# Kernel tuning notes

Measured on AMD Instinct MI355X. Metric: run time of the kernel, lower is better.

Reference implementation:

```python
import jax, jax.numpy as jnp
import numpy as np

ALPHA, BETA, GAMMA = 1.0, 1.0, 0.7
WIN = 11
C1 = 0.01 ** 2
C2 = 0.03 ** 2


def get_sobel_kernels(n1=1, n2=2, n3=2):
    a = np.asarray
    Sx = a([[[-n1, 0, n1], [-n2, 0, n2], [-n1, 0, n1]],
            [[-n2, 0, n2], [-n3 * n2, 0, n3 * n2], [-n2, 0, n2]],
            [[-n1, 0, n1], [-n2, 0, n2], [-n1, 0, n1]]])
    Sy = a([[[-n1, -n2, -n1], [0, 0, 0], [n1, n2, n1]],
            [[-n2, -n3 * n2, -n2], [0, 0, 0], [n2, n3 * n2, n2]],
            [[-n1, -n2, -n1], [0, 0, 0], [n1, n2, n1]]])
    Sz = a([[[-n1, -n2, -n1], [-n2, -n3 * n2, -n2], [-n1, -n2, -n1]],
            [[0, 0, 0], [0, 0, 0], [0, 0, 0]],
            [[n1, n2, n1], [n2, n3 * n2, n2], [n1, n2, n1]]])
    Sd11 = a([[[0, n1, n2], [-n1, 0, n1], [-n2, -n1, 0]],
              [[0, n2, n2 * n3], [-n2, 0, n2], [-n2 * n3, -n2, 0]],
              [[0, n1, n2], [-n1, 0, n1], [-n2, -n1, 0]]])
    Sd12 = a([[[-n2, -n1, 0], [-n1, 0, n1], [0, n1, n2]],
              [[-n2 * n3, -n2, 0], [-n2, 0, n2], [0, n2, n2 * n3]],
              [[-n2, -n1, 0], [-n1, 0, n1], [0, n1, n2]]])
    Sd21 = Sd11.T
    Sd22 = Sd12.T
    Sd31 = a([-S.T for S in Sd11.T])
    Sd32 = a([S.T for S in Sd12.T])
    return np.stack([Sx, Sy, Sz, Sd11, Sd12, Sd21, Sd22, Sd31, Sd32]).astype(np.float32)

# (9,1,3,3,3) fused sobel bank -- single grouped conv instead of 9 launches
SOBEL_W = jnp.asarray(get_sobel_kernels()[:, None])


def _gauss1d():
    g = jnp.exp(-(jnp.arange(WIN, dtype=jnp.float32) - WIN // 2) ** 2 / (2 * 1.5 ** 2))
    return g / g.sum()

G1D = _gauss1d()


def conv3d(x, w):
    return jax.lax.conv_general_dilated(
        x, w, window_strides=(1, 1, 1), padding='SAME',
        dimension_numbers=('NCDHW', 'OIDHW', 'NCDHW'))


def gauss_filter(x):
    # separable 11-tap gaussian along D, H, W (== full 11^3 window, zero-padded SAME)
    x = conv3d(x, G1D.reshape(1, 1, WIN, 1, 1))
    x = conv3d(x, G1D.reshape(1, 1, 1, WIN, 1))
    x = conv3d(x, G1D.reshape(1, 1, 1, 1, WIN))
    return x


def edge_map(img):
    # GradEdge3D.__call__ with a=1, C=1
    B, C, D, H, W = img.shape
    xp = jnp.pad(img, ((0, 0), (0, 0), (1, 1), (1, 1), (1, 1)), mode='reflect')
    g = conv3d(xp, SOBEL_W)                       # (B, 9, D+2, H+2, W+2)
    gm = jnp.sqrt(jnp.sum((g + 1e-6) ** 2 + 1e-6, axis=1))  # (B, D+2, H+2, W+2)
    gm = gm[:, 1:-1, 1:-1, 1:-1]
    norm = (gm - gm.min()) / (gm.max() - gm.min() + 1e-6)
    return norm.reshape(B, 1, D, H, W)


def ssim_value(pred, target):
    mu_p = gauss_filter(pred)
    mu_t = gauss_filter(target)
    mu_p2, mu_t2, mu_pt = mu_p ** 2, mu_t ** 2, mu_p * mu_t
    sig_p = gauss_filter(pred * pred) - mu_p2
    sig_t = gauss_filter(target * target) - mu_t2
    sig_pt = gauss_filter(pred * target) - mu_pt
    ssim_map = ((2 * mu_pt + C1) * (2 * sig_pt + C2)) / ((mu_p2 + mu_t2 + C1) * (sig_p + sig_t + C2))
    return 1.0 - ssim_map.mean()


def setup_inputs() -> dict:
    key = jax.random.key(0)
    k1, k2 = jax.random.split(key)
    shape = (2, 1, 128, 128, 128)
    return {
        'pred': jax.random.uniform(k1, shape, dtype=jnp.float32),
        'target': jax.random.uniform(k2, shape, dtype=jnp.float32),
    }


def reference(pred, target):
    loss_mse = jnp.mean((pred - target) ** 2)
    loss_ssim = ssim_value(pred, target)
    # GMELoss3D: lam_errors=[(1.0, L1Loss())], reduction='sum'
    loss_gme = 1e-6 + jnp.mean(jnp.abs(edge_map(pred) - edge_map(target)))
    total = ALPHA * loss_mse + BETA * loss_ssim + GAMMA * loss_gme
    return (total, loss_mse, loss_ssim, loss_gme)
```

## Files before the change

### kernel.cpp

```cpp
#include <hip/hip_runtime.h>


#define VOL 4194304
#define HV  2097152

typedef _Float16 h2 __attribute__((ext_vector_type(2)));
typedef _Float16 h4 __attribute__((ext_vector_type(4)));
typedef _Float16 h8 __attribute__((ext_vector_type(8)));

constexpr float GW[11] = {
    0.00102838f, 0.00759876f, 0.03600077f, 0.10936070f, 0.21300554f,
    0.26601173f,
    0.21300554f, 0.10936070f, 0.03600077f, 0.00759876f, 0.00102838f};



__device__ __forceinline__ void wblur_body(
    const float* __restrict__ p, const float* __restrict__ t,
    _Float16* __restrict__ A, double* __restrict__ mseB, const int bidx) {
  __shared__ float sr[2][138];
  __shared__ float dr[2][138];
  __shared__ float redw[256];
  const int tid = threadIdx.x;
  const int rl = tid >> 7;
  const int x  = tid & 127;
  const int rowBase = bidx << 4;
  if (x < 5)    { sr[rl][x] = 0.f;      dr[rl][x] = 0.f; }
  if (x >= 123) { sr[rl][10 + x] = 0.f; dr[rl][10 + x] = 0.f; }
  float pv = p[((rowBase + rl) << 7) + x];
  float tv = t[((rowBase + rl) << 7) + x];
  float msel = 0.f;
  h4* __restrict__ A4 = (h4*)A;
  for (int it = 0; it < 8; ++it) {
    const int row  = rowBase + (it << 1) + rl;
    const int base = row << 7;
    const float sv = pv + tv;
    const float dv = pv - tv;
    sr[rl][5 + x] = sv; dr[rl][5 + x] = dv;
    msel += dv * dv;
    __syncthreads();
    float pvN = 0.f, tvN = 0.f;
    if (it < 7) {
      const int baseN = (row + 2) << 7;
      pvN = p[baseN + x]; tvN = t[baseN + x];
    }
    float as = 0.f, ad = 0.f, ass = 0.f, add_ = 0.f;
#pragma unroll
    for (int k = 0; k < 11; ++k) {
      const float w = GW[k];
      const float a = sr[rl][x + k];
      const float b = dr[rl][x + k];
      const float wa = w * a;
      const float wb = w * b;
      as += wa; ad += wb;
      ass += wa * a; add_ += wb * b;
    }
    h4 o;
    o[0] = (_Float16)as;  o[1] = (_Float16)ad;
    o[2] = (_Float16)ass; o[3] = (_Float16)add_;
    A4[base + x] = o;
    __syncthreads();
    pv = pvN; tv = tvN;
  }
  redw[tid] = msel;
  __syncthreads();
  for (int s = 128; s > 0; s >>= 1) {
    if (tid < s) redw[tid] += redw[tid + s];
    __syncthreads();
  }
  if (tid == 0) atomicAdd(&mseB[(bidx & 63) << 3], (double)redw[0]);
}

__device__ __forceinline__ void sobel_body(
    const float* __restrict__ p, const float* __restrict__ t,
    _Float16* __restrict__ gmP, _Float16* __restrict__ gmT,
    unsigned int* __restrict__ ui, const int bx, const int by, const int bz) {
  __shared__ float sb[1296];
  __shared__ float rmin[256];
  __shared__ float rmax[256];
  const int tid = threadIdx.x;
  const int tx = tid & 15;
  const int ty = tid >> 4;
  const int x0 = bx << 4;
  const int y0 = by << 4;
  const int vol = bz >> 3;
  const int b   = (bz >> 2) & 1;
  const int z0  = (bz & 3) << 5;
  const float* __restrict__ img = vol ? t : p;
  _Float16* __restrict__ gm = vol ? gmT : gmP;
  const int vb = b << 21;

  const int ly1 = tid / 24, lx1 = tid % 24;
  const bool v1 = (lx1 < 18);
  int gy1 = y0 - 1 + ly1; gy1 = gy1 < 0 ? 1 : (gy1 > 127 ? 126 : gy1);
  int gx1 = x0 - 1 + lx1; gx1 = gx1 < 0 ? 1 : (gx1 > 127 ? 126 : gx1);
  const int off1 = (gy1 << 7) + gx1;
  const int s2i = tid + 256;
  const int ly2 = s2i / 24, lx2 = s2i % 24;
  const bool v2 = (s2i < 432) && (lx2 < 18);
  int gy2 = y0 - 1 + ly2; gy2 = gy2 < 0 ? 1 : (gy2 > 127 ? 126 : gy2);
  int gx2 = x0 - 1 + lx2; gx2 = gx2 < 0 ? 1 : (gx2 > 127 ? 126 : gx2);
  const int off2 = (gy2 << 7) + gx2;
  const int rb = ty * 24 + tx;
  const int gbase = vb + (z0 << 14) + ((y0 + ty) << 7) + (x0 + tx);

  float Y0[7], Y1[7], Y2[7];
  float rv1 = 0.f, rv2 = 0.f;
  float lmin = 3.4e38f, lmax = 0.f;

#define LOADR(ZS) {                                                         \
    const int zc_ = (ZS) > 127 ? 126 : (ZS);                                \
    const int za_ = vb + (zc_ << 14);                                       \
    if (v1) rv1 = img[za_ + off1];                                          \
    if (v2) rv2 = img[za_ + off2]; }

#define WRITELDS(BOFF) {                                                    \
    if (v1) sb[(BOFF) + tid] = rv1;                                         \
    if (v2) sb[(BOFF) + s2i] = rv2; }

#define COMPY(P) {                                                          \
    const int o_ = (P) * 432 + rb;                                          \
    const float r00 = sb[o_],      r01 = sb[o_ + 1],  r02 = sb[o_ + 2];     \
    const float r10 = sb[o_ + 24], r11 = sb[o_ + 25], r12 = sb[o_ + 26];    \
    const float r20 = sb[o_ + 48], r21 = sb[o_ + 49], r22 = sb[o_ + 50];    \
    const float dx0 = r02 - r00, dx1 = r12 - r10, dx2 = r22 - r20;          \
    const float ux0 = r00 + r01 + r02, ux1 = r10 + r11 + r12,               \
                ux2 = r20 + r21 + r22;                                      \
    const float sx0 = ux0 + r01, sx1 = ux1 + r11, sx2 = ux2 + r21;          \
    Y##P[1] = dx0 + dx1 + dx2;                                    \
    Y##P[0] = Y##P[1] + dx1;                                      \
    Y##P[2] = sx2 - sx0;                                          \
    Y##P[4] = sx0 + sx1 + sx2;                                    \
    Y##P[3] = Y##P[4] + sx1;                                      \
    Y##P[5] = ux2 - ux0;                                          \
    Y##P[6] = (ux0 + ux2) + 2.f * ux1; }

#define EMIT(I, P0, P1, P2) {                                               \
    const float E_ = Y##P0[0] + Y##P1[0] + Y##P2[0];                        \
    const float g1 = E_ + Y##P1[0];                                         \
    const float tA = Y##P0[1] + Y##P1[1] + Y##P2[1];                        \
    const float A_ = tA + Y##P1[1];                                         \
    const float D_ = Y##P0[2] + Y##P1[2] + Y##P2[2];                        \
    const float g2 = D_ + Y##P1[2];                                         \
    const float g3 = Y##P2[3] - Y##P0[3];                                   \
    const float C_ = Y##P2[4] - Y##P0[4];                                   \
    const float B_ = (Y##P0[5] + Y##P2[5]) + 2.f * Y##P1[5];                \
    const float F_ = Y##P2[6] - Y##P0[6];                                   \
    const float g4 = A_ - B_, g5 = A_ + B_;                                 \
    const float g6 = C_ - D_, g7 = C_ + D_;                                 \
    const float g8 = E_ - F_, g9 = E_ + F_;                                 \
    float ss_ = 9e-6f, t_;                                                  \
    t_ = g1 + 1e-6f; ss_ = fmaf(t_, t_, ss_);                               \
    t_ = g2 + 1e-6f; ss_ = fmaf(t_, t_, ss_);                               \
    t_ = g3 + 1e-6f; ss_ = fmaf(t_, t_, ss_);                               \
    t_ = g4 + 1e-6f; ss_ = fmaf(t_, t_, ss_);                               \
    t_ = g5 + 1e-6f; ss_ = fmaf(t_, t_, ss_);                               \
    t_ = g6 + 1e-6f; ss_ = fmaf(t_, t_, ss_);                               \
    t_ = g7 + 1e-6f; ss_ = fmaf(t_, t_, ss_);                               \
    t_ = g8 + 1e-6f; ss_ = fmaf(t_, t_, ss_);                               \
    t_ = g9 + 1e-6f; ss_ = fmaf(t_, t_, ss_);                               \
    const _Float16 gh = (_Float16)sqrtf(ss_);                               \
    gm[gbase + ((I) << 14)] = gh;                                           \
    const float gq = (float)gh;                                             \
    lmin = fminf(lmin, gq); lmax = fmaxf(lmax, gq); }

#define BODY(I, P0, P1, P2) {                                               \
    WRITELDS((P2) * 432);                                                   \
    LOADR(z0 + (I) + 2);                                                    \
    __syncthreads();                                                        \
    COMPY(P2);                                                              \
    EMIT(I, P0, P1, P2); }

  {
    const int zp = (z0 == 0) ? 1 : (z0 - 1);
    LOADR(zp);  WRITELDS(0);
    LOADR(z0);  WRITELDS(432);
    __syncthreads();
    COMPY(0);
    COMPY(1);
    LOADR(z0 + 1);
  }
  for (int ii = 0; ii < 30; ii += 3) {
    BODY(ii,     0, 1, 2);
    BODY(ii + 1, 1, 2, 0);
    BODY(ii + 2, 2, 0, 1);
  }
  BODY(30, 0, 1, 2);
  BODY(31, 1, 2, 0);

#undef BODY
#undef EMIT
#undef COMPY
#undef WRITELDS
#undef LOADR

  rmin[tid] = lmin; rmax[tid] = lmax;
  __syncthreads();
  for (int st = 128; st > 0; st >>= 1) {
    if (tid < st) {
      rmin[tid] = fminf(rmin[tid], rmin[tid + st]);
      rmax[tid] = fmaxf(rmax[tid], rmax[tid + st]);
    }
    __syncthreads();
  }
  if (tid == 0) {
    const int bin = (bx + (by << 3) + (bz << 6)) & 63;
    atomicMax(&ui[vol * 1024 + (bin << 4)], ~__float_as_uint(rmin[0]));
    atomicMax(&ui[2048 + vol * 1024 + (bin << 4)], __float_as_uint(rmax[0]));
  }
}

__device__ __forceinline__ void blury_body(
    const _Float16* __restrict__ A, _Float16* __restrict__ B,
    const int z, const int yseg, const int batch) {
  __shared__ h8 s[26][64];
  const int tid = threadIdx.x;
  const int y0 = yseg << 4;
  const h8* __restrict__ Ah = (const h8*)A;
  h8* __restrict__ Bh = (h8*)B;
  const int slice8 = (batch << 20) + (z << 13);
  for (int l = tid; l < 1664; l += 256) {
    const int row = l >> 6, xc = l & 63;
    const int y = y0 - 5 + row;
    h8 v{};
    if ((unsigned)y < 128u) v = Ah[slice8 + (y << 6) + xc];
    s[row][xc] = v;
  }
  __syncthreads();
  const int xc = tid & 63;
  const int yg = tid >> 6;
#pragma unroll
  for (int r = 0; r < 4; ++r) {
    const int yo = (yg << 2) + r;
    h8 acc{};
#pragma unroll
    for (int k = 0; k < 11; ++k) {
      const _Float16 w = (_Float16)GW[k];
      acc += w * s[yo + k][xc];
    }
    Bh[slice8 + ((y0 + yo) << 6) + xc] = acc;
  }
}

__device__ __forceinline__ void edge_body(
    const _Float16* __restrict__ gmP, const _Float16* __restrict__ gmT,
    const unsigned int* __restrict__ ui, double* __restrict__ absB,
    const int bidx) {
  __shared__ float rede[256];
  unsigned umnp = 0u, umnt = 0u, umxp = 0u, umxt = 0u;
  for (int j = 0; j < 64; ++j) {
    const unsigned a0 = ui[j << 4];
    const unsigned a1 = ui[1024 + (j << 4)];
    const unsigned a2 = ui[2048 + (j << 4)];
    const unsigned a3 = ui[3072 + (j << 4)];
    umnp = umnp > a0 ? umnp : a0;
    umnt = umnt > a1 ? umnt : a1;
    umxp = umxp > a2 ? umxp : a2;
    umxt = umxt > a3 ? umxt : a3;
  }
  const float mnp = __uint_as_float(~umnp);
  const float mnt = __uint_as_float(~umnt);
  const float mxp = __uint_as_float(umxp);
  const float mxt = __uint_as_float(umxt);
  const float scp = 1.f / (mxp - mnp + 1e-6f);
  const float sct = 1.f / (mxt - mnt + 1e-6f);
  const h8* __restrict__ gp = (const h8*)gmP;
  const h8* __restrict__ gt = (const h8*)gmT;
  float lsum = 0.f;
  const int base = bidx << 9;
#pragma unroll
  for (int i = 0; i < 2; ++i) {
    const int idx = base + (i << 8) + threadIdx.x;
    const h8 a = gp[idx];
    const h8 b = gt[idx];
#pragma unroll
    for (int j = 0; j < 8; ++j)
      lsum += fabsf(((float)a[j] - mnp) * scp - ((float)b[j] - mnt) * sct);
  }
  rede[threadIdx.x] = lsum;
  __syncthreads();
  for (int s = 128; s > 0; s >>= 1) {
    if (threadIdx.x < s) rede[threadIdx.x] += rede[threadIdx.x + s];
    __syncthreads();
  }
  if (threadIdx.x == 0)
    atomicAdd(&absB[(bidx & 63) << 3], (double)rede[0]);
}

__global__ __launch_bounds__(256) void k_fused_a(
    const float* __restrict__ p, const float* __restrict__ t,
    _Float16* __restrict__ A, double* __restrict__ mseB,
    _Float16* __restrict__ gmP, _Float16* __restrict__ gmT,
    unsigned int* __restrict__ ui) {
  const int bid = blockIdx.x;
  const int r3 = bid % 3;
  if (r3 < 2) {
    wblur_body(p, t, A, mseB, (bid / 3) * 2 + r3);
  } else {
    const int s = bid / 3;
    sobel_body(p, t, gmP, gmT, ui, s & 7, (s >> 3) & 7, s >> 6);
  }
}

__global__ __launch_bounds__(256) void k_fused_b(
    const _Float16* __restrict__ A, _Float16* __restrict__ B,
    const _Float16* __restrict__ gmP, const _Float16* __restrict__ gmT,
    const unsigned int* __restrict__ ui, double* __restrict__ absB) {
  const int bid = blockIdx.x;
  const int r3 = bid % 3;
  if (r3 < 2) {
    const int idx = (bid / 3) * 2 + r3;
    blury_body(A, B, idx & 127, (idx >> 7) & 7, idx >> 10);
  } else {
    edge_body(gmP, gmT, ui, absB, bid / 3);
  }
}

__global__ __launch_bounds__(256) void k_zblur_ssim(
    const _Float16* __restrict__ B, double* __restrict__ ssimB) {
  __shared__ h8 s[26][64];
  __shared__ float red[256];
  const int tid = threadIdx.x;
  const int y  = blockIdx.x;
  const int z0 = blockIdx.y << 4;
  const h8* __restrict__ Bh = (const h8*)B;
  const int col8 = (blockIdx.z << 20) + (y << 6);
  for (int l = tid; l < 1664; l += 256) {
    const int row = l >> 6, xc = l & 63;
    const int zz = z0 - 5 + row;
    h8 v{};
    if ((unsigned)zz < 128u) v = Bh[col8 + (zz << 13) + xc];
    s[row][xc] = v;
  }
  __syncthreads();
  const int xc = tid & 63;
  const int zg = tid >> 6;
  float lsum = 0.f;
#pragma unroll
  for (int r = 0; r < 4; ++r) {
    const int zo = (zg << 2) + r;
    h8 m{};
#pragma unroll
    for (int k = 0; k < 11; ++k) {
      const _Float16 w = (_Float16)GW[k];
      m += w * s[zo + k][xc];
    }
#pragma unroll
    for (int j = 0; j < 2; ++j) {
      const float mus = (float)m[4 * j + 0];
      const float mud = (float)m[4 * j + 1];
      const float ess = (float)m[4 * j + 2];
      const float edd = (float)m[4 * j + 3];
      const float S2 = mus * mus, D2 = mud * mud;
      const float num = ((S2 - D2) * 0.5f + 1e-4f) *
                        ((ess - edd - S2 + D2) * 0.5f + 9e-4f);
      const float den = ((S2 + D2) * 0.5f + 1e-4f) *
                        ((ess + edd - S2 - D2) * 0.5f + 9e-4f);
      lsum += num / den;
    }
  }
  red[tid] = lsum;
  __syncthreads();
  for (int st = 128; st > 0; st >>= 1) {
    if (tid < st) red[tid] += red[tid + st];
    __syncthreads();
  }
  if (tid == 0) {
    const int bin = (blockIdx.x + (blockIdx.y << 3) + blockIdx.z) & 63;
    atomicAdd(&ssimB[bin << 3], (double)red[0]);
  }
}

__global__ void k_final(const double* __restrict__ dbl, float* __restrict__ out) {
  if (threadIdx.x == 0 && blockIdx.x == 0) {
    double ms = 0.0, ss = 0.0, ab = 0.0;
    for (int j = 0; j < 64; ++j) {
      ms += dbl[j << 3];
      ss += dbl[512 + (j << 3)];
      ab += dbl[1024 + (j << 3)];
    }
    const double N = 4194304.0;
    const double mse   = ms / N;
    const double ssiml = 1.0 - ss / N;
    const double gme   = 1e-6 + ab / N;
    const double total = mse + ssiml + 0.7 * gme;
    out[0] = (float)total;
    out[1] = (float)mse;
    out[2] = (float)ssiml;
    out[3] = (float)gme;
  }
}

extern "C" void kernel_launch(void* const* d_in, const int* in_sizes, int n_in,
                              void* d_out, int out_size, void* d_ws, size_t ws_size,
                              hipStream_t stream) {
  const float* p = (const float*)d_in[0];
  const float* t = (const float*)d_in[1];
  _Float16* A = (_Float16*)d_ws;
  _Float16* B = A + (size_t)4 * VOL;
  char* accb = (char*)d_ws + (size_t)20 * VOL;
  double* dbl = (double*)accb;
  unsigned int* ui = (unsigned int*)(accb + 12288);
  _Float16* gmP = (_Float16*)((char*)d_ws + 88080384);
  _Float16* gmT = gmP + VOL;
  float* out = (float*)d_out;

  hipMemsetAsync(accb, 0, 28672, stream);
  k_fused_a<<<3072, 256, 0, stream>>>(p, t, A, dbl, gmP, gmT, ui);
  k_fused_b<<<3072, 256, 0, stream>>>(A, B, gmP, gmT, ui, dbl + 1024);
  k_zblur_ssim<<<dim3(128, 8, 2), 256, 0, stream>>>(B, dbl + 512);
  k_final<<<1, 64, 0, stream>>>(dbl, out);
}
```

Baseline: 150.7 us.

## Move edge-L1 work into z-blur kernel, share LDS pool, rework W-blur load

The edge-map L1 reduction blocks move out of the Y-blur kernel and are interleaved with the z-blur/SSIM kernel, so the Y-blur launch runs only its 2048 blur blocks. Shared memory in the fused first kernel now comes from one aliased pool across the W-blur and Sobel branches, which lowers per-block LDS use and may raise occupancy. The W-blur body now loads all 16 rows up front with a single barrier instead of looping two rows at a time with two barriers per step. This trades barrier count and LDS footprint for more live loads per thread and a different mix of work in each kernel.

```diff
diff --git a/kernel.cpp b/kernel.cpp
--- a/kernel.cpp
+++ b/kernel.cpp
@@ -17,39 +17,40 @@
 
 __device__ __forceinline__ void wblur_body(
     const float* __restrict__ p, const float* __restrict__ t,
-    _Float16* __restrict__ A, double* __restrict__ mseB, const int bidx) {
-  __shared__ float sr[2][138];
-  __shared__ float dr[2][138];
-  __shared__ float redw[256];
+    _Float16* __restrict__ A, double* __restrict__ mseB, const int bidx,
+    char* __restrict__ pool, float* __restrict__ redw) {
+  float (* __restrict__ sr)[138] = (float (*)[138])pool;
+  float (* __restrict__ dr)[138] = (float (*)[138])(pool + 8832);
   const int tid = threadIdx.x;
-  const int rl = tid >> 7;
-  const int x  = tid & 127;
-  const int rowBase = bidx << 4;
-  if (x < 5)    { sr[rl][x] = 0.f;      dr[rl][x] = 0.f; }
-  if (x >= 123) { sr[rl][10 + x] = 0.f; dr[rl][10 + x] = 0.f; }
-  float pv = p[((rowBase + rl) << 7) + x];
-  float tv = t[((rowBase + rl) << 7) + x];
+  const int gbase = bidx << 11;
+  if (tid < 160) {
+    const int r = tid / 10, j = tid % 10;
+    const int c = (j < 5) ? j : (128 + j);
+    sr[r][c] = 0.f; dr[r][c] = 0.f;
+  }
   float msel = 0.f;
+#pragma unroll
+  for (int i = 0; i < 8; ++i) {
+    const int v = (i << 8) + tid;
+    const float pv = p[gbase + v];
+    const float tv = t[gbase + v];
+    const float sv = pv + tv, dv = pv - tv;
+    sr[v >> 7][5 + (v & 127)] = sv;
+    dr[v >> 7][5 + (v & 127)] = dv;
+    msel += dv * dv;
+  }
+  __syncthreads();
   h4* __restrict__ A4 = (h4*)A;
-  for (int it = 0; it < 8; ++it) {
-    const int row  = rowBase + (it << 1) + rl;
-    const int base = row << 7;
-    const float sv = pv + tv;
-    const float dv = pv - tv;
-    sr[rl][5 + x] = sv; dr[rl][5 + x] = dv;
-    msel += dv * dv;
-    __syncthreads();
-    float pvN = 0.f, tvN = 0.f;
-    if (it < 7) {
-      const int baseN = (row + 2) << 7;
-      pvN = p[baseN + x]; tvN = t[baseN + x];
-    }
+#pragma unroll
+  for (int i = 0; i < 8; ++i) {
+    const int v = (i << 8) + tid;
+    const int row = v >> 7, x = v & 127;
     float as = 0.f, ad = 0.f, ass = 0.f, add_ = 0.f;
 #pragma unroll
     for (int k = 0; k < 11; ++k) {
       const float w = GW[k];
-      const float a = sr[rl][x + k];
-      const float b = dr[rl][x + k];
+      const float a = sr[row][x + k];
+      const float b = dr[row][x + k];
       const float wa = w * a;
       const float wb = w * b;
       as += wa; ad += wb;
@@ -58,9 +59,7 @@
     h4 o;
     o[0] = (_Float16)as;  o[1] = (_Float16)ad;
     o[2] = (_Float16)ass; o[3] = (_Float16)add_;
-    A4[base + x] = o;
-    __syncthreads();
-    pv = pvN; tv = tvN;
+    A4[gbase + v] = o;
   }
   redw[tid] = msel;
   __syncthreads();
@@ -74,10 +73,10 @@
 __device__ __forceinline__ void sobel_body(
     const float* __restrict__ p, const float* __restrict__ t,
     _Float16* __restrict__ gmP, _Float16* __restrict__ gmT,
-    unsigned int* __restrict__ ui, const int bx, const int by, const int bz) {
-  __shared__ float sb[1296];
-  __shared__ float rmin[256];
-  __shared__ float rmax[256];
+    unsigned int* __restrict__ ui, const int bx, const int by, const int bz,
+    char* __restrict__ pool, float* __restrict__ rmin) {
+  float* __restrict__ sb   = (float*)pool;
+  float* __restrict__ rmax = (float*)(pool + 5184);
   const int tid = threadIdx.x;
   const int tx = tid & 15;
   const int ty = tid >> 4;
@@ -245,8 +244,7 @@
 __device__ __forceinline__ void edge_body(
     const _Float16* __restrict__ gmP, const _Float16* __restrict__ gmT,
     const unsigned int* __restrict__ ui, double* __restrict__ absB,
-    const int bidx) {
-  __shared__ float rede[256];
+    const int bidx, float* __restrict__ rede) {
   unsigned umnp = 0u, umnt = 0u, umxp = 0u, umxt = 0u;
   for (int j = 0; j < 64; ++j) {
     const unsigned a0 = ui[j << 4];
@@ -292,39 +290,44 @@
     _Float16* __restrict__ A, double* __restrict__ mseB,
     _Float16* __restrict__ gmP, _Float16* __restrict__ gmT,
     unsigned int* __restrict__ ui) {
+  __shared__ __align__(16) char pool[17664];
+  __shared__ float redshared[256];
   const int bid = blockIdx.x;
   const int r3 = bid % 3;
   if (r3 < 2) {
-    wblur_body(p, t, A, mseB, (bid / 3) * 2 + r3);
+    wblur_body(p, t, A, mseB, (bid / 3) * 2 + r3, pool, redshared);
   } else {
     const int s = bid / 3;
-    sobel_body(p, t, gmP, gmT, ui, s & 7, (s >> 3) & 7, s >> 6);
+    sobel_body(p, t, gmP, gmT, ui, s & 7, (s >> 3) & 7, s >> 6,
+               pool, redshared);
   }
 }
 
 __global__ __launch_bounds__(256) void k_fused_b(
-    const _Float16* __restrict__ A, _Float16* __restrict__ B,
+    const _Float16* __restrict__ A, _Float16* __restrict__ B) {
+  const int idx = blockIdx.x;
+  blury_body(A, B, idx & 127, (idx >> 7) & 7, idx >> 10);
+}
+
+__global__ __launch_bounds__(256) void k_zblur_ssim(
+    const _Float16* __restrict__ B, double* __restrict__ ssimB,
     const _Float16* __restrict__ gmP, const _Float16* __restrict__ gmT,
     const unsigned int* __restrict__ ui, double* __restrict__ absB) {
-  const int bid = blockIdx.x;
-  const int r3 = bid % 3;
-  if (r3 < 2) {
-    const int idx = (bid / 3) * 2 + r3;
-    blury_body(A, B, idx & 127, (idx >> 7) & 7, idx >> 10);
-  } else {
-    edge_body(gmP, gmT, ui, absB, bid / 3);
-  }
-}
-
-__global__ __launch_bounds__(256) void k_zblur_ssim(
-    const _Float16* __restrict__ B, double* __restrict__ ssimB) {
   __shared__ h8 s[26][64];
   __shared__ float red[256];
   const int tid = threadIdx.x;
-  const int y  = blockIdx.x;
-  const int z0 = blockIdx.y << 4;
+  const int bid = blockIdx.x;
+  const int r3 = bid % 3;
+  if (r3 == 2) {
+    edge_body(gmP, gmT, ui, absB, bid / 3, red);
+    return;
+  }
+  const int idx = (bid / 3) * 2 + r3;
+  const int y = idx & 127;
+  const int z0 = ((idx >> 7) & 7) << 4;
+  const int batch = idx >> 10;
   const h8* __restrict__ Bh = (const h8*)B;
-  const int col8 = (blockIdx.z << 20) + (y << 6);
+  const int col8 = (batch << 20) + (y << 6);
   for (int l = tid; l < 1664; l += 256) {
     const int row = l >> 6, xc = l & 63;
     const int zz = z0 - 5 + row;
@@ -366,7 +369,7 @@
     __syncthreads();
   }
   if (tid == 0) {
-    const int bin = (blockIdx.x + (blockIdx.y << 3) + blockIdx.z) & 63;
+    const int bin = idx & 63;
     atomicAdd(&ssimB[bin << 3], (double)red[0]);
   }
 }
@@ -407,7 +410,7 @@
 
   hipMemsetAsync(accb, 0, 28672, stream);
   k_fused_a<<<3072, 256, 0, stream>>>(p, t, A, dbl, gmP, gmT, ui);
-  k_fused_b<<<3072, 256, 0, stream>>>(A, B, gmP, gmT, ui, dbl + 1024);
-  k_zblur_ssim<<<dim3(128, 8, 2), 256, 0, stream>>>(B, dbl + 512);
+  k_fused_b<<<2048, 256, 0, stream>>>(A, B);
+  k_zblur_ssim<<<3072, 256, 0, stream>>>(B, dbl + 512, gmP, gmT, ui, dbl + 1024);
   k_final<<<1, 64, 0, stream>>>(dbl, out);
 }
```

Result: no change. 149.4 us (-0.9%).
